# Kernel tuning notes

Measured on AMD Instinct MI355X. Metric: run time of the kernel, lower is better.

Reference implementation:

```python
import jax, jax.numpy as jnp
import numpy as np

N = 50000
D = 128
E = 600000
C = 128  # out_channels


def setup_inputs() -> dict:
    key = jax.random.key(0)
    ks = jax.random.split(key, 8)
    x = jax.random.normal(ks[0], (N, D), dtype=jnp.float32)
    edge_index = jax.random.randint(ks[1], (2, E), 0, N, dtype=jnp.int64)
    s = 1.0 / np.sqrt(D)
    # layer 1: PyG GraphConv = lin_rel (with bias) on aggregated neighbors + lin_root (no bias) on self
    W1_rel = jax.random.uniform(ks[2], (C, D), jnp.float32, -s, s)
    b1_rel = jax.random.uniform(ks[3], (C,), jnp.float32, -s, s)
    W1_root = jax.random.uniform(ks[4], (C, D), jnp.float32, -s, s)
    s2 = 1.0 / np.sqrt(C)
    W2_rel = jax.random.uniform(ks[5], (C, C), jnp.float32, -s2, s2)
    b2_rel = jax.random.uniform(ks[6], (C,), jnp.float32, -s2, s2)
    W2_root = jax.random.uniform(ks[7], (C, C), jnp.float32, -s2, s2)
    return {"x": x, "edge_index": edge_index,
            "W1_rel": W1_rel, "b1_rel": b1_rel, "W1_root": W1_root,
            "W2_rel": W2_rel, "b2_rel": b2_rel, "W2_root": W2_root}


def _graph_conv(x, src, tgt, W_rel, b_rel, W_root):
    # sum-aggregate source-node features onto targets, then linear transforms
    agg = jax.ops.segment_sum(x[src], tgt, num_segments=N)  # [N, d_in]
    return agg @ W_rel.T + b_rel + x @ W_root.T


def reference(x, edge_index, W1_rel, b1_rel, W1_root, W2_rel, b2_rel, W2_root):
    src, tgt = edge_index[0], edge_index[1]
    h = jax.nn.relu(_graph_conv(x, src, tgt, W1_rel, b1_rel, W1_root))
    h = jax.nn.relu(_graph_conv(h, src, tgt, W2_rel, b2_rel, W2_root))
    return h
```

## Files before the change

### kernel.cpp

```cpp
#include <hip/hip_runtime.h>
#include <hip/hip_bf16.h>

#define DD 128

typedef __attribute__((ext_vector_type(8))) short bf16x8;
typedef __attribute__((ext_vector_type(4))) float f32x4;
typedef __attribute__((ext_vector_type(8))) unsigned short us8;
typedef unsigned short ushort_t;
typedef unsigned int uint_t;

__device__ inline ushort_t f2bf(float f) {
    __hip_bfloat16 h = __float2bfloat16(f);
    union { __hip_bfloat16 h; ushort_t u; } cv;
    cv.h = h;
    return cv.u;
}
__device__ inline float bf2f(uint_t lo16) {
    union { uint_t i; float f; } v;
    v.i = lo16 << 16;
    return v.f;
}
__device__ inline void conv8(const float* __restrict__ in, ushort_t* __restrict__ outp) {
    const float4 va = *(const float4*)in;
    const float4 vb = *(const float4*)(in + 4);
    ushort_t r[8];
    r[0] = f2bf(va.x); r[1] = f2bf(va.y); r[2] = f2bf(va.z); r[3] = f2bf(va.w);
    r[4] = f2bf(vb.x); r[5] = f2bf(vb.y); r[6] = f2bf(vb.z); r[7] = f2bf(vb.w);
    *(bf16x8*)outp = *(bf16x8*)r;
}


__global__ __launch_bounds__(256) void zero_convx(int* __restrict__ pos, int n4, int zb,
                                                  const float* __restrict__ x,
                                                  ushort_t* __restrict__ xb, int n8) {
    if ((int)blockIdx.x < zb) {
        int i = blockIdx.x * 256 + threadIdx.x;
        if (i < n4) ((int4*)pos)[i] = make_int4(0, 0, 0, 0);
    } else {
        int i = (blockIdx.x - zb) * 256 + threadIdx.x;
        if (i < n8) conv8(x + (size_t)i * 8, xb + (size_t)i * 8);
    }
}


__global__ __launch_bounds__(256) void count_rank(const int* __restrict__ tgt,
                                                  int* __restrict__ pos,
                                                  ushort_t* __restrict__ erank, int e) {
    int i = blockIdx.x * 256 + threadIdx.x;
    int e8 = e >> 3;
    if (i < e8) {
        int4 t0 = ((const int4*)tgt)[i * 2];
        int4 t1 = ((const int4*)tgt)[i * 2 + 1];
        us8 r;
        r[0] = (ushort_t)atomicAdd(&pos[t0.x], 1);
        r[1] = (ushort_t)atomicAdd(&pos[t0.y], 1);
        r[2] = (ushort_t)atomicAdd(&pos[t0.z], 1);
        r[3] = (ushort_t)atomicAdd(&pos[t0.w], 1);
        r[4] = (ushort_t)atomicAdd(&pos[t1.x], 1);
        r[5] = (ushort_t)atomicAdd(&pos[t1.y], 1);
        r[6] = (ushort_t)atomicAdd(&pos[t1.z], 1);
        r[7] = (ushort_t)atomicAdd(&pos[t1.w], 1);
        ((us8*)erank)[i] = r;
    }
    if (i == 0)
        for (int j = e8 * 8; j < e; ++j)
            erank[j] = (ushort_t)atomicAdd(&pos[tgt[j]], 1);
}


__global__ __launch_bounds__(1024) void scan_part(const int* __restrict__ cnt,
                                                  int* __restrict__ off,
                                                  int* __restrict__ bsum, int n) {
    const int t = threadIdx.x;
    const int i = blockIdx.x * 1024 + t;
    const int v = (i < n) ? cnt[i] : 0;
    const int lane = t & 63, wv = t >> 6;
    int s = v;
#pragma unroll
    for (int d = 1; d < 64; d <<= 1) {
        int o = __shfl_up(s, d, 64);
        if (lane >= d) s += o;
    }
    __shared__ int wsum[16];
    if (lane == 63) wsum[wv] = s;
    __syncthreads();
    int woff = 0;
    for (int k = 0; k < wv; ++k) woff += wsum[k];
    if (i < n) off[i] = woff + s - v;
    if (t == 1023) bsum[blockIdx.x] = woff + s;
}


__global__ __launch_bounds__(1024) void scan_final_convw(int* __restrict__ off,
                                                         const int* __restrict__ bsum,
                                                         int n, int nb,
                                                         const float* __restrict__ a,
                                                         const float* __restrict__ b,
                                                         const float* __restrict__ c,
                                                         const float* __restrict__ d,
                                                         ushort_t* __restrict__ wb) {
    const int blk = blockIdx.x;
    if (blk < nb) {
        int pre = 0;
        for (int k = 0; k < blk; ++k) pre += bsum[k];
        const int i = blk * 1024 + threadIdx.x;
        if (i < n) off[i] += pre;
        if (blk == nb - 1 && threadIdx.x == 0) {
            int tot = pre;
            for (int k = blk; k < nb; ++k) tot += bsum[k];
            off[n] = tot;
        }
    } else {
        int k = (blk - nb) * 1024 + threadIdx.x;
        if (k >= 8192) return;
        const float* p = (k < 2048) ? a : (k < 4096) ? b : (k < 6144) ? c : d;
        conv8(p + (size_t)(k & 2047) * 8, wb + (size_t)k * 8);
    }
}


__global__ __launch_bounds__(256) void fill_scatter(const int* __restrict__ src,
                                                    const int* __restrict__ tgt,
                                                    const int* __restrict__ off,
                                                    const ushort_t* __restrict__ erank,
                                                    ushort_t* __restrict__ esrc, int e) {
    int i = blockIdx.x * 256 + threadIdx.x;
    int e8 = e >> 3;
    if (i < e8) {
        int4 t0 = ((const int4*)tgt)[i * 2];
        int4 t1 = ((const int4*)tgt)[i * 2 + 1];
        int4 s0 = ((const int4*)src)[i * 2];
        int4 s1 = ((const int4*)src)[i * 2 + 1];
        us8 r = ((const us8*)erank)[i];
        int o0 = off[t0.x], o1 = off[t0.y], o2 = off[t0.z], o3 = off[t0.w];
        int o4 = off[t1.x], o5 = off[t1.y], o6 = off[t1.z], o7 = off[t1.w];
        esrc[o0 + r[0]] = (ushort_t)s0.x;
        esrc[o1 + r[1]] = (ushort_t)s0.y;
        esrc[o2 + r[2]] = (ushort_t)s0.z;
        esrc[o3 + r[3]] = (ushort_t)s0.w;
        esrc[o4 + r[4]] = (ushort_t)s1.x;
        esrc[o5 + r[5]] = (ushort_t)s1.y;
        esrc[o6 + r[6]] = (ushort_t)s1.z;
        esrc[o7 + r[7]] = (ushort_t)s1.w;
    }
    if (i == 0)
        for (int j = e8 * 8; j < e; ++j)
            esrc[off[tgt[j]] + erank[j]] = (ushort_t)src[j];
}


template<int K>
__device__ inline void gath(const ushort_t* __restrict__ xrow,
                            const ushort_t* __restrict__ esrc, int j,
                            float& ax, float& ay) {
    int s[K];
    uint_t v[K];
#pragma unroll
    for (int k = 0; k < K; ++k) s[k] = esrc[j + k];
#pragma unroll
    for (int k = 0; k < K; ++k) v[k] = *(const uint_t*)(xrow + (size_t)s[k] * DD);
#pragma unroll
    for (int k = 0; k < K; ++k) {
        ax += bf2f(v[k] & 0xffffu);
        ay += bf2f(v[k] >> 16);
    }
}

__global__ __launch_bounds__(256) void gather_agg_bf16(const ushort_t* __restrict__ xin,
                                                       const int* __restrict__ off,
                                                       const ushort_t* __restrict__ esrc,
                                                       ushort_t* __restrict__ agg, int n) {
    const int lane = threadIdx.x & 63;
    const int node = blockIdx.x * 4 + (threadIdx.x >> 6);
    if (node >= n) return;
    const int beg = off[node], end = off[node + 1];
    const ushort_t* xrow = xin + lane * 2;
    float ax = 0.f, ay = 0.f;
    int j = beg;
    for (; j + 8 <= end; j += 8) gath<8>(xrow, esrc, j, ax, ay);
    if (j + 4 <= end) { gath<4>(xrow, esrc, j, ax, ay); j += 4; }
    if (j + 2 <= end) { gath<2>(xrow, esrc, j, ax, ay); j += 2; }
    if (j < end)      { gath<1>(xrow, esrc, j, ax, ay); }
    uint_t r = ((uint_t)f2bf(ay) << 16) | (uint_t)f2bf(ax);
    *(uint_t*)(agg + (size_t)node * DD + lane * 2) = r;
}

template<bool OUT_BF16>
__global__ __launch_bounds__(256) void gemm_mfma(
    const ushort_t* Aagg, const ushort_t* __restrict__ Aroot,
    const ushort_t* __restrict__ Wrel, const ushort_t* __restrict__ Wroot,
    const float* __restrict__ bias, void* outv, int n)
{
    const int wave = threadIdx.x >> 6;
    const int lane = threadIdx.x & 63;
    const int m = lane & 15;
    const int kg = lane >> 4;
    const int rbase = blockIdx.x * 64 + wave * 16;
    if (rbase >= n) return;
    const size_t aoff = (size_t)(rbase + m) * DD + kg * 8;

    f32x4 acc[8];
#pragma unroll
    for (int j = 0; j < 8; ++j) acc[j] = (f32x4){0.f, 0.f, 0.f, 0.f};

#pragma unroll
    for (int k0 = 0; k0 < DD; k0 += 32) {
        bf16x8 aA = *(const bf16x8*)(Aagg + aoff + k0);
        bf16x8 aR = *(const bf16x8*)(Aroot + aoff + k0);
#pragma unroll
        for (int j = 0; j < 8; ++j) {
            bf16x8 bL = *(const bf16x8*)(Wrel + (size_t)(j * 16 + m) * DD + kg * 8 + k0);
            bf16x8 bR = *(const bf16x8*)(Wroot + (size_t)(j * 16 + m) * DD + kg * 8 + k0);
            acc[j] = __builtin_amdgcn_mfma_f32_16x16x32_bf16(aA, bL, acc[j], 0, 0, 0);
            acc[j] = __builtin_amdgcn_mfma_f32_16x16x32_bf16(aR, bR, acc[j], 0, 0, 0);
        }
    }

    const int orow = rbase + kg * 4;
#pragma unroll
    for (int j = 0; j < 8; ++j) {
        const int col = j * 16 + m;
        const float bv = bias[col];
#pragma unroll
        for (int i = 0; i < 4; ++i) {
            float v = acc[j][i] + bv;
            v = v > 0.f ? v : 0.f;
            if (OUT_BF16)
                ((ushort_t*)outv)[(size_t)(orow + i) * DD + col] = f2bf(v);
            else
                ((float*)outv)[(size_t)(orow + i) * DD + col] = v;
        }
    }
}

extern "C" void kernel_launch(void* const* d_in, const int* in_sizes, int n_in,
                              void* d_out, int out_size, void* d_ws, size_t ws_size,
                              hipStream_t stream) {
    const float* x = (const float*)d_in[0];
    const int* ei = (const int*)d_in[1];
    const float* W1rel = (const float*)d_in[2];
    const float* b1 = (const float*)d_in[3];
    const float* W1root = (const float*)d_in[4];
    const float* W2rel = (const float*)d_in[5];
    const float* b2 = (const float*)d_in[6];
    const float* W2root = (const float*)d_in[7];
    float* out = (float*)d_out;

    const int n = in_sizes[0] / DD;
    const int e = in_sizes[1] / 2;
    const int* src = ei;
    const int* tgt = ei + e;
    const int nb = (n + 1023) / 1024;
    const int n8 = n * DD / 8;
    const int zb = (n / 4 + 255) / 256;

    char* ws = (char*)d_ws;
    int* off  = (int*)ws;
    int* bsum = (int*)(ws + 200064);
    int* pos  = (int*)(ws + 200320);
    ushort_t* wb = (ushort_t*)(ws + 200320);
    ushort_t* esrc = (ushort_t*)(ws + 400384);
    ushort_t* erank = (ushort_t*)(ws + 1600384);
    ushort_t* aggb = (ushort_t*)(ws + 2800640);
    ushort_t* xb = (ushort_t*)(ws + 15600640);

    zero_convx<<<zb + (n8 + 255) / 256, 256, 0, stream>>>(pos, n / 4, zb, x, xb, n8);
    count_rank<<<(e / 8 + 255) / 256, 256, 0, stream>>>(tgt, pos, erank, e);
    scan_part<<<nb, 1024, 0, stream>>>(pos, off, bsum, n);
    scan_final_convw<<<nb + 8, 1024, 0, stream>>>(off, bsum, n, nb,
                                                  W1rel, W1root, W2rel, W2root, wb);
    fill_scatter<<<(e / 8 + 255) / 256, 256, 0, stream>>>(src, tgt, off, erank, esrc, e);

    gather_agg_bf16<<<(n + 3) / 4, 256, 0, stream>>>(xb, off, esrc, aggb, n);
    gemm_mfma<true><<<(n + 63) / 64, 256, 0, stream>>>(aggb, xb, wb, wb + 16384, b1, aggb, n);

    gather_agg_bf16<<<(n + 3) / 4, 256, 0, stream>>>(aggb, off, esrc, xb, n);
    gemm_mfma<false><<<(n + 63) / 64, 256, 0, stream>>>(xb, aggb, wb + 32768, wb + 49152, b2, out, n);
}
```

Measured before the change: 175.0 us.

## Fuse neighbor gather-aggregation into MFMA GEMM via shared-memory tile

The separate gather_agg kernel is merged into the GEMM kernel. Each wave now sums neighbor features for 16 nodes one after another and writes them into an LDS tile. The MFMA GEMM then reads its A operand from that tile instead of from global memory. This removes the write and re-read of the aggregated bf16 buffer and two kernel launches. The cost is far fewer concurrent waves doing the latency-bound gather, and the GEMM cannot start until the whole block has finished gathering.

```diff
diff --git a/kernel.cpp b/kernel.cpp
--- a/kernel.cpp
+++ b/kernel.cpp
@@ -166,38 +166,44 @@
     }
 }
 
-__global__ __launch_bounds__(256) void gather_agg_bf16(const ushort_t* __restrict__ xin,
-                                                       const int* __restrict__ off,
-                                                       const ushort_t* __restrict__ esrc,
-                                                       ushort_t* __restrict__ agg, int n) {
-    const int lane = threadIdx.x & 63;
-    const int node = blockIdx.x * 4 + (threadIdx.x >> 6);
-    if (node >= n) return;
-    const int beg = off[node], end = off[node + 1];
-    const ushort_t* xrow = xin + lane * 2;
-    float ax = 0.f, ay = 0.f;
-    int j = beg;
-    for (; j + 8 <= end; j += 8) gath<8>(xrow, esrc, j, ax, ay);
-    if (j + 4 <= end) { gath<4>(xrow, esrc, j, ax, ay); j += 4; }
-    if (j + 2 <= end) { gath<2>(xrow, esrc, j, ax, ay); j += 2; }
-    if (j < end)      { gath<1>(xrow, esrc, j, ax, ay); }
-    uint_t r = ((uint_t)f2bf(ay) << 16) | (uint_t)f2bf(ax);
-    *(uint_t*)(agg + (size_t)node * DD + lane * 2) = r;
-}
-
 template<bool OUT_BF16>
-__global__ __launch_bounds__(256) void gemm_mfma(
-    const ushort_t* Aagg, const ushort_t* __restrict__ Aroot,
-    const ushort_t* __restrict__ Wrel, const ushort_t* __restrict__ Wroot,
+__global__ __launch_bounds__(256) void fused_gather_gemm(
+    const ushort_t* __restrict__ xin,
+    const int* __restrict__ off,
+    const ushort_t* __restrict__ esrc,
+    const ushort_t* __restrict__ Aroot,
+    const ushort_t* __restrict__ Wrel,
+    const ushort_t* __restrict__ Wroot,
     const float* __restrict__ bias, void* outv, int n)
 {
+    __shared__ ushort_t sA[64][136];
     const int wave = threadIdx.x >> 6;
     const int lane = threadIdx.x & 63;
+    const int rbase = blockIdx.x * 64 + wave * 16;
+
+    if (rbase < n) {
+        const ushort_t* xrow = xin + lane * 2;
+#pragma unroll 1
+        for (int i = 0; i < 16; ++i) {
+            const int nd = rbase + i;
+            const int beg = off[nd], end = off[nd + 1];
+            float ax = 0.f, ay = 0.f;
+            int j = beg;
+            for (; j + 8 <= end; j += 8) gath<8>(xrow, esrc, j, ax, ay);
+            if (j + 4 <= end) { gath<4>(xrow, esrc, j, ax, ay); j += 4; }
+            if (j + 2 <= end) { gath<2>(xrow, esrc, j, ax, ay); j += 2; }
+            if (j < end)      { gath<1>(xrow, esrc, j, ax, ay); }
+            uint_t r = ((uint_t)f2bf(ay) << 16) | (uint_t)f2bf(ax);
+            *(uint_t*)&sA[wave * 16 + i][lane * 2] = r;
+        }
+    }
+    __syncthreads();
+    if (rbase >= n) return;
+
     const int m = lane & 15;
     const int kg = lane >> 4;
-    const int rbase = blockIdx.x * 64 + wave * 16;
-    if (rbase >= n) return;
-    const size_t aoff = (size_t)(rbase + m) * DD + kg * 8;
+    const ushort_t* aLds = &sA[wave * 16 + m][kg * 8];
+    const size_t roff = (size_t)(rbase + m) * DD + kg * 8;
 
     f32x4 acc[8];
 #pragma unroll
@@ -205,8 +211,8 @@
 
 #pragma unroll
     for (int k0 = 0; k0 < DD; k0 += 32) {
-        bf16x8 aA = *(const bf16x8*)(Aagg + aoff + k0);
-        bf16x8 aR = *(const bf16x8*)(Aroot + aoff + k0);
+        bf16x8 aA = *(const bf16x8*)(aLds + k0);
+        bf16x8 aR = *(const bf16x8*)(Aroot + roff + k0);
 #pragma unroll
         for (int j = 0; j < 8; ++j) {
             bf16x8 bL = *(const bf16x8*)(Wrel + (size_t)(j * 16 + m) * DD + kg * 8 + k0);
@@ -271,9 +277,8 @@
                                                   W1rel, W1root, W2rel, W2root, wb);
     fill_scatter<<<(e / 8 + 255) / 256, 256, 0, stream>>>(src, tgt, off, erank, esrc, e);
 
-    gather_agg_bf16<<<(n + 3) / 4, 256, 0, stream>>>(xb, off, esrc, aggb, n);
-    gemm_mfma<true><<<(n + 63) / 64, 256, 0, stream>>>(aggb, xb, wb, wb + 16384, b1, aggb, n);
-
-    gather_agg_bf16<<<(n + 3) / 4, 256, 0, stream>>>(aggb, off, esrc, xb, n);
-    gemm_mfma<false><<<(n + 63) / 64, 256, 0, stream>>>(xb, aggb, wb + 32768, wb + 49152, b2, out, n);
-}
+    fused_gather_gemm<true><<<(n + 63) / 64, 256, 0, stream>>>(
+        xb, off, esrc, xb, wb, wb + 16384, b1, aggb, n);
+    fused_gather_gemm<false><<<(n + 63) / 64, 256, 0, stream>>>(
+        aggb, off, esrc, aggb, wb + 32768, wb + 49152, b2, out, n);
+}
```

Result: slower. 193.2 us (+10.4%).
